# Optimization experiments

Hardware: AMD Instinct MI355X
Metric: run time of the kernel (lower is better)

The kernel has to match this reference:

```python
import jax, jax.numpy as jnp
import numpy as np

INPUT_DIM = 1024
NUM_TARGETS = 128
BATCH = 32768


def setup_inputs() -> dict:
    key = jax.random.key(0)
    kx, kw, kb = jax.random.split(key, 3)
    x = jax.random.normal(kx, (BATCH, INPUT_DIM), dtype=jnp.float32)
    # Fused view of num_targets independent nn.Linear(input_dim, 1) layers:
    # column t of W / entry t of b are the weights/bias of layer t.
    bound = 1.0 / np.sqrt(INPUT_DIM)  # torch Linear default init range
    W = jax.random.uniform(kw, (INPUT_DIM, NUM_TARGETS), minval=-bound, maxval=bound, dtype=jnp.float32)
    b = jax.random.uniform(kb, (NUM_TARGETS,), minval=-bound, maxval=bound, dtype=jnp.float32)
    return {"x": x, "W": W, "b": b}


def reference(x, W, b):
    # Equivalent to concatenating sigmoid(Linear_t(x)) over t along last dim:
    # one fused matmul [B,D]x[D,T] + bias + sigmoid.
    return jax.nn.sigmoid(x @ W + b)
```

## Files before the change

### kernel.cpp

```cpp
#include <hip/hip_runtime.h>
#include <hip/hip_bf16.h>


typedef __bf16 bf16x8 __attribute__((ext_vector_type(8)));
typedef float  f32x4  __attribute__((ext_vector_type(4)));

#define DIM   1024
#define NT    128
#define BATCH 32768

__global__ __launch_bounds__(256) void prep_w(const float* __restrict__ W,
                                              __bf16* __restrict__ wsW) {
    int idx = blockIdx.x * 256 + threadIdx.x;
    int j = idx & 7;
    int l = (idx >> 3) & 63;
    int c = (idx >> 9) & 7;
    int s = idx >> 12;
    int k = s * 32 + (l >> 4) * 8 + j;
    int n = c * 16 + (l & 15);
    wsW[idx] = (__bf16)W[k * NT + n];
}

__device__ __forceinline__ bf16x8 cvt_bf16x8(float4 a0, float4 a1) {
    bf16x8 af;
    af[0] = (__bf16)a0.x; af[1] = (__bf16)a0.y;
    af[2] = (__bf16)a0.z; af[3] = (__bf16)a0.w;
    af[4] = (__bf16)a1.x; af[5] = (__bf16)a1.y;
    af[6] = (__bf16)a1.z; af[7] = (__bf16)a1.w;
    return af;
}

__global__ __launch_bounds__(512, 2) void gemm_bias_sigmoid(
        const float* __restrict__ x,
        const __hip_bfloat16* __restrict__ wsWh,
        const float* __restrict__ bias,
        float* __restrict__ out) {
    const bf16x8* __restrict__ wsW8 = (const bf16x8*)wsWh;
    __shared__ bf16x8 ldsW[8192];

    const int tid  = threadIdx.x;
    const int lane = tid & 63;
    const int wave = tid >> 6;
    const int q    = lane >> 4;
    const int r    = lane & 15;
    const int row0 = blockIdx.x * 128 + wave * 16;

    const float* xA = x + (size_t)(row0 + r) * DIM + q * 8;

    f32x4 acc[8];
#pragma unroll
    for (int c = 0; c < 8; ++c)
        acc[c] = (f32x4){0.f, 0.f, 0.f, 0.f};

    float4 A[4][2];
#pragma unroll
    for (int i = 0; i < 4; ++i) {
        A[i][0] = *(const float4*)(xA + (size_t)i * 32);
        A[i][1] = *(const float4*)(xA + (size_t)i * 32 + 4);
    }

#pragma unroll
    for (int i = 0; i < 16; ++i)
        ldsW[tid + i * 512] = wsW8[tid + i * 512];
    __syncthreads();

#pragma unroll
    for (int h = 0; h < 2; ++h) {
        if (h == 1) {
            __syncthreads();
#pragma unroll
            for (int i = 0; i < 16; ++i)
                ldsW[tid + i * 512] = wsW8[8192 + tid + i * 512];
            __syncthreads();
        }
#pragma unroll
        for (int sl = 0; sl < 16; ++sl) {
            const int s   = h * 16 + sl;
            const int buf = s & 3;

            const bf16x8 af = cvt_bf16x8(A[buf][0], A[buf][1]);

            if (s + 4 < 32) {
                A[buf][0] = *(const float4*)(xA + (size_t)(s + 4) * 32);
                A[buf][1] = *(const float4*)(xA + (size_t)(s + 4) * 32 + 4);
            }

#pragma unroll
            for (int c = 0; c < 8; ++c) {
                const bf16x8 bf = ldsW[(sl * 8 + c) * 64 + lane];
                acc[c] = __builtin_amdgcn_mfma_f32_16x16x32_bf16(af, bf, acc[c], 0, 0, 0);
            }
        }
    }

#pragma unroll
    for (int c = 0; c < 8; ++c) {
        const float bv = bias[c * 16 + r];
#pragma unroll
        for (int reg = 0; reg < 4; ++reg) {
            const int row = row0 + q * 4 + reg;
            float v = acc[c][reg] + bv;
            v = 1.0f / (1.0f + __expf(-v));
            out[(size_t)row * NT + c * 16 + r] = v;
        }
    }
}

extern "C" void kernel_launch(void* const* d_in, const int* in_sizes, int n_in,
                              void* d_out, int out_size, void* d_ws, size_t ws_size,
                              hipStream_t stream) {
    const float* x = (const float*)d_in[0];
    const float* W = (const float*)d_in[1];
    const float* b = (const float*)d_in[2];
    float* out     = (float*)d_out;
    __bf16* wsW    = (__bf16*)d_ws;

    prep_w<<<DIM * NT / 256, 256, 0, stream>>>(W, wsW);
    gemm_bias_sigmoid<<<BATCH / 128, 512, 0, stream>>>(
        x, (const __hip_bfloat16*)wsW, b, out);
}
```

Baseline: 211.8 us.

## Stage x and W through double-buffered LDS with async global-to-LDS loads

Restructures the GEMM main loop so W tiles are streamed into a double-buffered LDS region with global_load_lds (async DMA), and x rows are loaded coalesced by the whole block, converted to bf16, and staged into padded double-buffered LDS tiles. Loads of the next k-chunk overlap the MFMAs on the current one, replacing the two blocking W loads and the per-lane strided x loads. LDS use grows to about 100KB per block, which likely caps occupancy at one block per CU, and there are more barriers per iteration.

```diff
diff --git a/kernel.cpp b/kernel.cpp
--- a/kernel.cpp
+++ b/kernel.cpp
@@ -3,11 +3,18 @@
 
 
 typedef __bf16 bf16x8 __attribute__((ext_vector_type(8)));
+typedef __bf16 bf16x4 __attribute__((ext_vector_type(4)));
 typedef float  f32x4  __attribute__((ext_vector_type(4)));
+typedef unsigned int u32_as1 __attribute__((address_space(1)));
+typedef unsigned int u32_as3 __attribute__((address_space(3)));
 
 #define DIM   1024
 #define NT    128
 #define BATCH 32768
+
+#define WBUF(b) ((unsigned)(b) * 32768u)
+#define ABUF(b) (65536u + (unsigned)(b) * 17408u)
+#define LDS_TOTAL (65536 + 2 * 17408)
 
 __global__ __launch_bounds__(256) void prep_w(const float* __restrict__ W,
                                               __bf16* __restrict__ wsW) {
@@ -21,84 +28,98 @@
     wsW[idx] = (__bf16)W[k * NT + n];
 }
 
-__device__ __forceinline__ bf16x8 cvt_bf16x8(float4 a0, float4 a1) {
-    bf16x8 af;
-    af[0] = (__bf16)a0.x; af[1] = (__bf16)a0.y;
-    af[2] = (__bf16)a0.z; af[3] = (__bf16)a0.w;
-    af[4] = (__bf16)a1.x; af[5] = (__bf16)a1.y;
-    af[6] = (__bf16)a1.z; af[7] = (__bf16)a1.w;
-    return af;
-}
-
-__global__ __launch_bounds__(512, 2) void gemm_bias_sigmoid(
+__global__ __launch_bounds__(512) void gemm_bias_sigmoid(
         const float* __restrict__ x,
         const __hip_bfloat16* __restrict__ wsWh,
         const float* __restrict__ bias,
         float* __restrict__ out) {
+    __shared__ __align__(16) unsigned char lds[LDS_TOTAL];
     const bf16x8* __restrict__ wsW8 = (const bf16x8*)wsWh;
-    __shared__ bf16x8 ldsW[8192];
 
     const int tid  = threadIdx.x;
     const int lane = tid & 63;
     const int wave = tid >> 6;
     const int q    = lane >> 4;
     const int r    = lane & 15;
-    const int row0 = blockIdx.x * 128 + wave * 16;
+    const int row0 = blockIdx.x * 128;
 
-    const float* xA = x + (size_t)(row0 + r) * DIM + q * 8;
+    const int arow = tid >> 4;
+    const int kpos = (tid & 15) * 4;
+    const float* xA = x + (size_t)(row0 + arow) * DIM + kpos;
 
     f32x4 acc[8];
 #pragma unroll
     for (int c = 0; c < 8; ++c)
         acc[c] = (f32x4){0.f, 0.f, 0.f, 0.f};
 
-    float4 A[4][2];
+    float4 aA[4], aB[4];
+
+    auto wdma = [&](int ph) {
 #pragma unroll
-    for (int i = 0; i < 4; ++i) {
-        A[i][0] = *(const float4*)(xA + (size_t)i * 32);
-        A[i][1] = *(const float4*)(xA + (size_t)i * 32 + 4);
+        for (int i = 0; i < 4; ++i) {
+            const bf16x8* g = wsW8 + ((size_t)ph * 2048 + i * 512 + tid);
+            __builtin_amdgcn_global_load_lds(
+                (const u32_as1*)g,
+                (u32_as3*)(lds + WBUF(ph & 1) + (unsigned)((i * 512 + tid) * 16)),
+                16, 0, 0);
+        }
+    };
+    auto loadA = [&](float4* dst, int c) {
+        const float* ap = xA + (size_t)c * 64;
+        dst[0] = *(const float4*)ap;
+        dst[1] = *(const float4*)(ap + 32 * DIM);
+        dst[2] = *(const float4*)(ap + 64 * DIM);
+        dst[3] = *(const float4*)(ap + 96 * DIM);
+    };
+    auto writeA = [&](const float4* src, int b) {
+#pragma unroll
+        for (int i = 0; i < 4; ++i) {
+            bf16x4 v;
+            v[0] = (__bf16)src[i].x; v[1] = (__bf16)src[i].y;
+            v[2] = (__bf16)src[i].z; v[3] = (__bf16)src[i].w;
+            *(bf16x4*)(lds + ABUF(b) +
+                       (unsigned)(arow + 32 * i) * 136u + (unsigned)(kpos * 2)) = v;
+        }
+    };
+    auto comp = [&](int p, int wb) {
+#pragma unroll
+        for (int sl = 0; sl < 2; ++sl) {
+            const bf16x8 af = *(const bf16x8*)(lds + ABUF(p) +
+                (unsigned)(wave * 16 + r) * 136u + (unsigned)(sl * 64 + q * 16));
+#pragma unroll
+            for (int cc = 0; cc < 8; ++cc) {
+                const bf16x8 bf = *(const bf16x8*)(lds + WBUF(wb) +
+                    (unsigned)(((p * 2 + sl) * 8 + cc) * 1024 + lane * 16));
+                acc[cc] = __builtin_amdgcn_mfma_f32_16x16x32_bf16(af, bf, acc[cc], 0, 0, 0);
+            }
+        }
+    };
+
+    wdma(0);
+    loadA(aA, 0);
+    writeA(aA, 0);
+    loadA(aA, 1);
+    __syncthreads();
+
+    for (int t = 0; t < 8; ++t) {
+        if (t < 7) wdma(t + 1);
+        if (t < 7) loadA(aB, 2 * t + 2);
+        comp(0, t & 1);
+        writeA(aA, 1);
+        __syncthreads();
+        if (t < 7) loadA(aA, 2 * t + 3);
+        comp(1, t & 1);
+        if (t < 7) writeA(aB, 0);
+        __syncthreads();
     }
 
-#pragma unroll
-    for (int i = 0; i < 16; ++i)
-        ldsW[tid + i * 512] = wsW8[tid + i * 512];
-    __syncthreads();
-
-#pragma unroll
-    for (int h = 0; h < 2; ++h) {
-        if (h == 1) {
-            __syncthreads();
-#pragma unroll
-            for (int i = 0; i < 16; ++i)
-                ldsW[tid + i * 512] = wsW8[8192 + tid + i * 512];
-            __syncthreads();
-        }
-#pragma unroll
-        for (int sl = 0; sl < 16; ++sl) {
-            const int s   = h * 16 + sl;
-            const int buf = s & 3;
-
-            const bf16x8 af = cvt_bf16x8(A[buf][0], A[buf][1]);
-
-            if (s + 4 < 32) {
-                A[buf][0] = *(const float4*)(xA + (size_t)(s + 4) * 32);
-                A[buf][1] = *(const float4*)(xA + (size_t)(s + 4) * 32 + 4);
-            }
-
-#pragma unroll
-            for (int c = 0; c < 8; ++c) {
-                const bf16x8 bf = ldsW[(sl * 8 + c) * 64 + lane];
-                acc[c] = __builtin_amdgcn_mfma_f32_16x16x32_bf16(af, bf, acc[c], 0, 0, 0);
-            }
-        }
-    }
-
+    const int wrow = row0 + wave * 16;
 #pragma unroll
     for (int c = 0; c < 8; ++c) {
         const float bv = bias[c * 16 + r];
 #pragma unroll
         for (int reg = 0; reg < 4; ++reg) {
-            const int row = row0 + q * 4 + reg;
+            const int row = wrow + q * 4 + reg;
             float v = acc[c][reg] + bv;
             v = 1.0f / (1.0f + __expf(-v));
             out[(size_t)row * NT + c * 16 + r] = v;
```

Measured after the change: 211.0 us. Within noise of the previous version (-0.4%).
